# Performance work log

Measured on AMD Instinct MI355X. Metric: run time of the kernel, lower is better.

The kernel has to match this reference:

```python
import jax, jax.numpy as jnp
import numpy as np

N = 8192
E = 262144

def gcn_conv(x, W, b, row, col, w):
    # PyG GCNConv with self-loops already appended to (row, col, w).
    h = x @ W                                   # [N, out]
    deg = jax.ops.segment_sum(w, col, num_segments=N)
    dinv = jnp.where(deg > 0, jax.lax.rsqrt(deg), 0.0)
    norm = dinv[row] * w * dinv[col]            # [E+N]
    out = jax.ops.segment_sum(norm[:, None] * h[row], col, num_segments=N)
    return out + b

def setup_inputs() -> dict:
    key = jax.random.key(0)
    ks = jax.random.split(key, 10)
    return {
        "x": jax.random.normal(ks[0], (N, 512), jnp.float32),
        "edge_index": jax.random.randint(ks[1], (2, E), 0, N, jnp.int64),
        "edge_weight": jax.random.uniform(ks[2], (E,), jnp.float32),
        "noise": jax.random.normal(ks[3], (N, 64), jnp.float32),
        "W1": jax.random.normal(ks[4], (512, 256), jnp.float32) * 0.05,
        "b1": jnp.zeros((256,), jnp.float32),
        "W2": jax.random.normal(ks[5], (256, 256), jnp.float32) * 0.05,
        "b2": jnp.zeros((256,), jnp.float32),
        "Wm": jax.random.normal(ks[6], (256, 64), jnp.float32) * 0.05,
        "bm": jnp.zeros((64,), jnp.float32),
        "Ws": jax.random.normal(ks[7], (256, 64), jnp.float32) * 0.05,
        "bs": jnp.zeros((64,), jnp.float32),
    }

def reference(x, edge_index, edge_weight, noise, W1, b1, W2, b2, Wm, bm, Ws, bs):
    # add self-loops once (weight 1.0), shared by all GCN layers
    loop = jnp.arange(N, dtype=edge_index.dtype)
    row = jnp.concatenate([edge_index[0], loop])
    col = jnp.concatenate([edge_index[1], loop])
    w = jnp.concatenate([edge_weight, jnp.ones((N,), edge_weight.dtype)])

    h = jax.nn.relu(gcn_conv(x, W1, b1, row, col, w))
    h = jax.nn.relu(gcn_conv(h, W2, b2, row, col, w))
    mean = jax.nn.relu(gcn_conv(h, Wm, bm, row, col, w))
    log_std = jax.nn.relu(gcn_conv(h, Ws, bs, row, col, w))
    z = noise * jnp.exp(log_std) + mean          # [N, 64]
    adj = jax.nn.sigmoid(z @ z.T)                # [N, N]
    return jnp.triu(adj, k=1)
```

## Files before the change

### kernel.cpp

```cpp
#include <hip/hip_runtime.h>
#include <hip/hip_bf16.h>

#define NN 8192
#define NE 262144

typedef __attribute__((ext_vector_type(8))) short bf16x8;
typedef __attribute__((ext_vector_type(4))) float f32x4;

__global__ __launch_bounds__(256) void k_init(float* __restrict__ deg, int* __restrict__ counts,
                                              int* __restrict__ cnt2) {
  int i = blockIdx.x * 256 + threadIdx.x;
  if (i < NN) { deg[i] = 1.0f; counts[i] = 0; cnt2[i] = 0; }
}

__global__ __launch_bounds__(256) void k_count(const int* __restrict__ ei, const float* __restrict__ w,
                                               float* __restrict__ deg, int* __restrict__ counts) {
  int e = blockIdx.x * 256 + threadIdx.x;
  if (e < NE) {
    int c = ei[NE + e];
    atomicAdd(&deg[c], w[e]);
    atomicAdd(&counts[c], 1);
  }
}

__global__ __launch_bounds__(1024) void k_scan(const int* __restrict__ counts, int* __restrict__ offs) {
  __shared__ int part[1024];
  int t = threadIdx.x;
  int base = t * 8;
  int local[8];
  int s = 0;
#pragma unroll
  for (int j = 0; j < 8; ++j) { local[j] = counts[base + j]; s += local[j]; }
  part[t] = s;
  __syncthreads();
  for (int off = 1; off < 1024; off <<= 1) {
    int v = (t >= off) ? part[t - off] : 0;
    __syncthreads();
    part[t] += v;
    __syncthreads();
  }
  int run = (t > 0) ? part[t - 1] : 0;
#pragma unroll
  for (int j = 0; j < 8; ++j) { offs[base + j] = run; run += local[j]; }
  if (t == 1023) offs[NN] = run;
}

__global__ __launch_bounds__(256) void k_scatter(const int* __restrict__ ei, const float* __restrict__ w,
                                                 const float* __restrict__ deg, const int* __restrict__ offs,
                                                 int* __restrict__ cnt2, int* __restrict__ csr_row,
                                                 float* __restrict__ csr_val) {
  int e = blockIdx.x * 256 + threadIdx.x;
  if (e < NE) {
    int r = ei[e], c = ei[NE + e];
    int slot = offs[c] + atomicAdd(&cnt2[c], 1);
    csr_row[slot] = r;
    csr_val[slot] = rsqrtf(deg[r]) * w[e] * rsqrtf(deg[c]);
  }
}

__global__ __launch_bounds__(256) void k_gemm(const float* __restrict__ A, const float* __restrict__ B,
                                              float* __restrict__ C, int M, int K, int Nc) {
  __shared__ float As[16][68];
  __shared__ float Bs[16][64];
  int t = threadIdx.x;
  int tx = t & 15, ty = t >> 4;
  int m0 = blockIdx.y * 64, n0 = blockIdx.x * 64;
  int la_r = t >> 2;
  int la_c = (t & 3) * 4;
  int lb_r = t >> 4;
  int lb_c = (t & 15) * 4;
  const float* Aptr = A + (size_t)(m0 + la_r) * K + la_c;
  const float* Bptr = B + (size_t)lb_r * Nc + n0 + lb_c;
  float acc[4][4] = {};
  for (int k0 = 0; k0 < K; k0 += 16) {
    float4 av = *(const float4*)(Aptr + k0);
    float4 bv = *(const float4*)(Bptr + (size_t)k0 * Nc);
    __syncthreads();
    As[la_c + 0][la_r] = av.x;
    As[la_c + 1][la_r] = av.y;
    As[la_c + 2][la_r] = av.z;
    As[la_c + 3][la_r] = av.w;
    *(float4*)&Bs[lb_r][lb_c] = bv;
    __syncthreads();
#pragma unroll
    for (int kk = 0; kk < 16; ++kk) {
      f32x4 a4 = *(const f32x4*)&As[kk][ty * 4];
      f32x4 b4 = *(const f32x4*)&Bs[kk][tx * 4];
#pragma unroll
      for (int i = 0; i < 4; ++i)
#pragma unroll
        for (int j = 0; j < 4; ++j)
          acc[i][j] = fmaf(a4[i], b4[j], acc[i][j]);
    }
  }
#pragma unroll
  for (int i = 0; i < 4; ++i) {
    f32x4 v = {acc[i][0], acc[i][1], acc[i][2], acc[i][3]};
    *(f32x4*)&C[(size_t)(m0 + ty * 4 + i) * Nc + n0 + tx * 4] = v;
  }
}

template <int D>
__global__ __launch_bounds__(256) void k_agg(const float* __restrict__ t, const float* __restrict__ deg,
                                             const int* __restrict__ csr_row, const float* __restrict__ csr_val,
                                             const int* __restrict__ offs, const float* __restrict__ bias,
                                             float* __restrict__ outb) {
  constexpr int V = D / 64;
  __shared__ int   srow[256];
  __shared__ float sval[256];
  __shared__ float sacc[4][D];
  int c = blockIdx.x;
  int tid = threadIdx.x;
  int w = tid >> 6, lane = tid & 63;
  int d0 = lane * V;
  float acc[V];
#pragma unroll
  for (int j = 0; j < V; ++j) acc[j] = 0.0f;
  int s0 = offs[c], s1 = offs[c + 1];
  for (int base = s0; base < s1; base += 256) {
    int cnt = s1 - base; if (cnt > 256) cnt = 256;
    __syncthreads();
    if (tid < cnt) { srow[tid] = csr_row[base + tid]; sval[tid] = csr_val[base + tid]; }
    __syncthreads();
    for (int s = w; s < cnt; s += 4) {
      int r = srow[s];
      float v = sval[s];
      const float* p = t + (size_t)r * D + d0;
      if constexpr (V == 4) {
        float4 pv = *(const float4*)p;
        acc[0] = fmaf(v, pv.x, acc[0]);
        acc[1] = fmaf(v, pv.y, acc[1]);
        acc[2] = fmaf(v, pv.z, acc[2]);
        acc[3] = fmaf(v, pv.w, acc[3]);
      } else {
        float2 pv = *(const float2*)p;
        acc[0] = fmaf(v, pv.x, acc[0]);
        acc[1] = fmaf(v, pv.y, acc[1]);
      }
    }
  }
#pragma unroll
  for (int j = 0; j < V; ++j) sacc[w][d0 + j] = acc[j];
  __syncthreads();
  if (tid < 64) {
    float di = rsqrtf(deg[c]);
    float selfw = di * di;
#pragma unroll
    for (int j = 0; j < V; ++j) {
      int d = tid * V + j;
      float a = sacc[0][d] + sacc[1][d] + sacc[2][d] + sacc[3][d];
      a = fmaf(selfw, t[(size_t)c * D + d], a);
      outb[(size_t)c * D + d] = fmaxf(a + bias[d], 0.0f);
    }
  }
}

__global__ __launch_bounds__(256) void k_cat(const float* __restrict__ Wm, const float* __restrict__ Wsw,
                                             const float* __restrict__ bm, const float* __restrict__ bsv,
                                             float* __restrict__ Wcat, float* __restrict__ bcat) {
  int idx = blockIdx.x * 256 + threadIdx.x;
  if (idx < 256 * 128) {
    int k = idx >> 7, c = idx & 127;
    Wcat[idx] = (c < 64) ? Wm[k * 64 + c] : Wsw[k * 64 + (c - 64)];
  } else if (idx < 256 * 128 + 128) {
    int c = idx - 256 * 128;
    bcat[c] = (c < 64) ? bm[c] : bsv[c - 64];
  }
}

__global__ __launch_bounds__(256) void k_z(const float* __restrict__ gms, const float* __restrict__ noise,
                                           __hip_bfloat16* __restrict__ zh, __hip_bfloat16* __restrict__ zl) {
  int idx = blockIdx.x * 256 + threadIdx.x;
  int i = idx >> 6, k = idx & 63;
  float mean = gms[(size_t)i * 128 + k];
  float ls = gms[(size_t)i * 128 + 64 + k];
  float z = noise[idx] * __expf(ls) + mean;
  __hip_bfloat16 h = __float2bfloat16(z);
  zh[idx] = h;
  zl[idx] = __float2bfloat16(z - __bfloat162float(h));
}

__global__ __launch_bounds__(256) void k_final(const short* __restrict__ zh, const short* __restrict__ zl,
                                               float* __restrict__ out) {
  int ti = blockIdx.y, tj = blockIdx.x;
  int ri0 = ti * 128, cj0 = tj * 128;
  if (tj < ti) {
    f32x4 zz = {};
    int tr = threadIdx.x >> 5;
    int tc = (threadIdx.x & 31) << 2;
    float* base = out + (size_t)(ri0 + tr) * NN + cj0 + tc;
#pragma unroll
    for (int rr = 0; rr < 128; rr += 8)
      *(f32x4*)(base + (size_t)rr * NN) = zz;
    return;
  }
  int wv = threadIdx.x >> 6;
  int lane = threadIdx.x & 63;
  int wr = wv >> 1, wc = wv & 1;
  int lr = lane & 15;
  int lk = (lane >> 4) << 3;
  int arow = ri0 + wr * 64 + lr;
  int brow = cj0 + wc * 64 + lr;

  bf16x8 ah[4][2], al[4][2];
#pragma unroll
  for (int rb = 0; rb < 4; ++rb)
#pragma unroll
    for (int ks = 0; ks < 2; ++ks) {
      int o = (arow + rb * 16) * 64 + ks * 32 + lk;
      ah[rb][ks] = *(const bf16x8*)(zh + o);
      al[rb][ks] = *(const bf16x8*)(zl + o);
    }
  f32x4 acc[4][4] = {};
#pragma unroll
  for (int cb = 0; cb < 4; ++cb) {
    bf16x8 bh[2], bl[2];
#pragma unroll
    for (int ks = 0; ks < 2; ++ks) {
      int o = (brow + cb * 16) * 64 + ks * 32 + lk;
      bh[ks] = *(const bf16x8*)(zh + o);
      bl[ks] = *(const bf16x8*)(zl + o);
    }
#pragma unroll
    for (int rb = 0; rb < 4; ++rb) {
      f32x4 c = acc[rb][cb];
#pragma unroll
      for (int ks = 0; ks < 2; ++ks) {
        c = __builtin_amdgcn_mfma_f32_16x16x32_bf16(ah[rb][ks], bh[ks], c, 0, 0, 0);
        c = __builtin_amdgcn_mfma_f32_16x16x32_bf16(ah[rb][ks], bl[ks], c, 0, 0, 0);
        c = __builtin_amdgcn_mfma_f32_16x16x32_bf16(al[rb][ks], bh[ks], c, 0, 0, 0);
      }
      acc[rb][cb] = c;
    }
  }
  int orow = ri0 + wr * 64 + ((lane >> 4) << 2);
  int ocol = cj0 + wc * 64 + (lane & 15);
#pragma unroll
  for (int rb = 0; rb < 4; ++rb)
#pragma unroll
    for (int cb = 0; cb < 4; ++cb)
#pragma unroll
      for (int r = 0; r < 4; ++r) {
        int row = orow + rb * 16 + r;
        int col = ocol + cb * 16;
        float v = acc[rb][cb][r];
        float sg = 1.0f / (1.0f + __expf(-v));
        out[(size_t)row * NN + col] = (col > row) ? sg : 0.0f;
      }
}

extern "C" void kernel_launch(void* const* d_in, const int* in_sizes, int n_in,
                              void* d_out, int out_size, void* d_ws, size_t ws_size,
                              hipStream_t stream) {
  (void)in_sizes; (void)n_in; (void)out_size; (void)ws_size;
  const float* x     = (const float*)d_in[0];
  const int*   ei    = (const int*)d_in[1];
  const float* ew    = (const float*)d_in[2];
  const float* noise = (const float*)d_in[3];
  const float* W1    = (const float*)d_in[4];
  const float* b1    = (const float*)d_in[5];
  const float* W2    = (const float*)d_in[6];
  const float* b2    = (const float*)d_in[7];
  const float* Wm    = (const float*)d_in[8];
  const float* bm    = (const float*)d_in[9];
  const float* Wsw   = (const float*)d_in[10];
  const float* bsv   = (const float*)d_in[11];
  float* out = (float*)d_out;

  char* wsb = (char*)d_ws;
  size_t off = 0;
  auto bump = [&](size_t bytes) -> void* {
    void* p = wsb + off;
    off += (bytes + 255) & ~(size_t)255;
    return p;
  };
  float* deg     = (float*)bump((size_t)NN * 4);
  int*   counts  = (int*)bump((size_t)NN * 4);
  int*   offs    = (int*)bump((size_t)(NN + 1) * 4);
  int*   cnt2    = (int*)bump((size_t)NN * 4);
  int*   csr_row = (int*)bump((size_t)NE * 4);
  float* csr_val = (float*)bump((size_t)NE * 4);
  float* bufA    = (float*)bump((size_t)NN * 256 * 4);
  float* bufB    = (float*)bump((size_t)NN * 256 * 4);
  float* bufC    = (float*)bump((size_t)NN * 128 * 4);
  float* bufG    = (float*)bump((size_t)NN * 128 * 4);
  float* Wcat    = (float*)bump((size_t)256 * 128 * 4);
  float* bcat    = (float*)bump((size_t)128 * 4);
  __hip_bfloat16* zh = (__hip_bfloat16*)bump((size_t)NN * 64 * 2);
  __hip_bfloat16* zl = (__hip_bfloat16*)bump((size_t)NN * 64 * 2);

  k_init<<<NN / 256, 256, 0, stream>>>(deg, counts, cnt2);
  k_count<<<NE / 256, 256, 0, stream>>>(ei, ew, deg, counts);
  k_scan<<<1, 1024, 0, stream>>>(counts, offs);
  k_scatter<<<NE / 256, 256, 0, stream>>>(ei, ew, deg, offs, cnt2, csr_row, csr_val);

  k_gemm<<<dim3(4, 128), 256, 0, stream>>>(x, W1, bufA, NN, 512, 256);
  k_agg<256><<<NN, 256, 0, stream>>>(bufA, deg, csr_row, csr_val, offs, b1, bufB);
  k_gemm<<<dim3(4, 128), 256, 0, stream>>>(bufB, W2, bufA, NN, 256, 256);
  k_agg<256><<<NN, 256, 0, stream>>>(bufA, deg, csr_row, csr_val, offs, b2, bufB);
  k_cat<<<129, 256, 0, stream>>>(Wm, Wsw, bm, bsv, Wcat, bcat);
  k_gemm<<<dim3(2, 128), 256, 0, stream>>>(bufB, Wcat, bufC, NN, 256, 128);
  k_agg<128><<<NN, 256, 0, stream>>>(bufC, deg, csr_row, csr_val, offs, bcat, bufG);
  k_z<<<NN * 64 / 256, 256, 0, stream>>>(bufG, noise, zh, zl);
  k_final<<<dim3(64, 64), 256, 0, stream>>>((const short*)zh, (const short*)zl, out);
}
```

Baseline: 274.0 us.

## Replace FP32 SIMT GEMMs with split-bf16 MFMA GEMMs and fused split outputs

Replaces the shared-memory FP32 FMA GEMM with a matrix-core kernel that uses three bf16 MFMA products (hi*hi, hi*lo, lo*hi) to approximate FP32 accuracy. Inputs are pre-split into hi/lo bf16 halves: x and the weights via new split kernels, and hidden activations directly inside the aggregation epilogue. The aim is to move the GEMM FLOPs onto the matrix cores. The cost is extra split passes, double-width bf16 operand traffic, and direct global loads without LDS staging, which may underuse bandwidth. Buffers are also aliased to reuse workspace.

After: 281.8 us. +2.8%, slower.

```diff
diff --git a/kernel.cpp b/kernel.cpp
--- a/kernel.cpp
+++ b/kernel.cpp
@@ -58,53 +58,100 @@
   }
 }
 
-__global__ __launch_bounds__(256) void k_gemm(const float* __restrict__ A, const float* __restrict__ B,
-                                              float* __restrict__ C, int M, int K, int Nc) {
-  __shared__ float As[16][68];
-  __shared__ float Bs[16][64];
-  int t = threadIdx.x;
-  int tx = t & 15, ty = t >> 4;
+__global__ __launch_bounds__(256) void k_splitX(const float* __restrict__ x,
+                                                __hip_bfloat16* __restrict__ xh,
+                                                __hip_bfloat16* __restrict__ xl) {
+  size_t i = ((size_t)blockIdx.x * 256 + threadIdx.x) * 4;
+  f32x4 v = *(const f32x4*)(x + i);
+#pragma unroll
+  for (int j = 0; j < 4; ++j) {
+    __hip_bfloat16 h = __float2bfloat16(v[j]);
+    xh[i + j] = h;
+    xl[i + j] = __float2bfloat16(v[j] - __bfloat162float(h));
+  }
+}
+
+__global__ __launch_bounds__(256) void k_splitW(const float* __restrict__ W,
+                                                __hip_bfloat16* __restrict__ WhT,
+                                                __hip_bfloat16* __restrict__ WlT, int K, int Nc) {
+  int idx = blockIdx.x * 256 + threadIdx.x;
+  if (idx < K * Nc) {
+    int k = idx / Nc, n = idx - k * Nc;
+    float v = W[idx];
+    __hip_bfloat16 h = __float2bfloat16(v);
+    WhT[(size_t)n * K + k] = h;
+    WlT[(size_t)n * K + k] = __float2bfloat16(v - __bfloat162float(h));
+  }
+}
+
+__global__ __launch_bounds__(256) void k_splitWcat(const float* __restrict__ Wm, const float* __restrict__ Wsw,
+                                                   const float* __restrict__ bm, const float* __restrict__ bsv,
+                                                   __hip_bfloat16* __restrict__ WhT,
+                                                   __hip_bfloat16* __restrict__ WlT,
+                                                   float* __restrict__ bcat) {
+  int idx = blockIdx.x * 256 + threadIdx.x;
+  int n = idx >> 8, k = idx & 255;
+  float v = (n < 64) ? Wm[k * 64 + n] : Wsw[k * 64 + (n - 64)];
+  __hip_bfloat16 h = __float2bfloat16(v);
+  WhT[idx] = h;
+  WlT[idx] = __float2bfloat16(v - __bfloat162float(h));
+  if (blockIdx.x == 0 && threadIdx.x < 128)
+    bcat[threadIdx.x] = (threadIdx.x < 64) ? bm[threadIdx.x] : bsv[threadIdx.x - 64];
+}
+
+__global__ __launch_bounds__(256) void k_gemm_mfma(const short* __restrict__ Ah, const short* __restrict__ Al,
+                                                   const short* __restrict__ BhT, const short* __restrict__ BlT,
+                                                   float* __restrict__ C, int K, int Nc) {
   int m0 = blockIdx.y * 64, n0 = blockIdx.x * 64;
-  int la_r = t >> 2;
-  int la_c = (t & 3) * 4;
-  int lb_r = t >> 4;
-  int lb_c = (t & 15) * 4;
-  const float* Aptr = A + (size_t)(m0 + la_r) * K + la_c;
-  const float* Bptr = B + (size_t)lb_r * Nc + n0 + lb_c;
-  float acc[4][4] = {};
-  for (int k0 = 0; k0 < K; k0 += 16) {
-    float4 av = *(const float4*)(Aptr + k0);
-    float4 bv = *(const float4*)(Bptr + (size_t)k0 * Nc);
-    __syncthreads();
-    As[la_c + 0][la_r] = av.x;
-    As[la_c + 1][la_r] = av.y;
-    As[la_c + 2][la_r] = av.z;
-    As[la_c + 3][la_r] = av.w;
-    *(float4*)&Bs[lb_r][lb_c] = bv;
-    __syncthreads();
-#pragma unroll
-    for (int kk = 0; kk < 16; ++kk) {
-      f32x4 a4 = *(const f32x4*)&As[kk][ty * 4];
-      f32x4 b4 = *(const f32x4*)&Bs[kk][tx * 4];
-#pragma unroll
-      for (int i = 0; i < 4; ++i)
-#pragma unroll
-        for (int j = 0; j < 4; ++j)
-          acc[i][j] = fmaf(a4[i], b4[j], acc[i][j]);
-    }
-  }
-#pragma unroll
-  for (int i = 0; i < 4; ++i) {
-    f32x4 v = {acc[i][0], acc[i][1], acc[i][2], acc[i][3]};
-    *(f32x4*)&C[(size_t)(m0 + ty * 4 + i) * Nc + n0 + tx * 4] = v;
-  }
-}
-
-template <int D>
+  int wv = threadIdx.x >> 6, lane = threadIdx.x & 63;
+  int wr = wv >> 1, wc = wv & 1;
+  int lr = lane & 15, lk8 = (lane >> 4) << 3;
+  int arow = m0 + wr * 32 + lr;
+  int bcol = n0 + wc * 32 + lr;
+  f32x4 acc[2][2] = {};
+  for (int k0 = 0; k0 < K; k0 += 32) {
+    bf16x8 ah[2], al[2], bh[2], bl[2];
+#pragma unroll
+    for (int rb = 0; rb < 2; ++rb) {
+      size_t o = (size_t)(arow + rb * 16) * K + k0 + lk8;
+      ah[rb] = *(const bf16x8*)(Ah + o);
+      al[rb] = *(const bf16x8*)(Al + o);
+    }
+#pragma unroll
+    for (int cb = 0; cb < 2; ++cb) {
+      size_t o = (size_t)(bcol + cb * 16) * K + k0 + lk8;
+      bh[cb] = *(const bf16x8*)(BhT + o);
+      bl[cb] = *(const bf16x8*)(BlT + o);
+    }
+#pragma unroll
+    for (int rb = 0; rb < 2; ++rb)
+#pragma unroll
+      for (int cb = 0; cb < 2; ++cb) {
+        f32x4 c = acc[rb][cb];
+        c = __builtin_amdgcn_mfma_f32_16x16x32_bf16(ah[rb], bh[cb], c, 0, 0, 0);
+        c = __builtin_amdgcn_mfma_f32_16x16x32_bf16(ah[rb], bl[cb], c, 0, 0, 0);
+        c = __builtin_amdgcn_mfma_f32_16x16x32_bf16(al[rb], bh[cb], c, 0, 0, 0);
+        acc[rb][cb] = c;
+      }
+  }
+  int orow = m0 + wr * 32 + ((lane >> 4) << 2);
+  int ocol = n0 + wc * 32 + (lane & 15);
+#pragma unroll
+  for (int rb = 0; rb < 2; ++rb)
+#pragma unroll
+    for (int cb = 0; cb < 2; ++cb)
+#pragma unroll
+      for (int r = 0; r < 4; ++r)
+        C[(size_t)(orow + rb * 16 + r) * Nc + ocol + cb * 16] = acc[rb][cb][r];
+}
+
+template <int D, bool SPLIT>
 __global__ __launch_bounds__(256) void k_agg(const float* __restrict__ t, const float* __restrict__ deg,
                                              const int* __restrict__ csr_row, const float* __restrict__ csr_val,
                                              const int* __restrict__ offs, const float* __restrict__ bias,
-                                             float* __restrict__ outb) {
+                                             float* __restrict__ outf,
+                                             __hip_bfloat16* __restrict__ outh,
+                                             __hip_bfloat16* __restrict__ outl) {
   constexpr int V = D / 64;
   __shared__ int   srow[256];
   __shared__ float sval[256];
@@ -150,21 +197,15 @@
       int d = tid * V + j;
       float a = sacc[0][d] + sacc[1][d] + sacc[2][d] + sacc[3][d];
       a = fmaf(selfw, t[(size_t)c * D + d], a);
-      outb[(size_t)c * D + d] = fmaxf(a + bias[d], 0.0f);
-    }
-  }
-}
-
-__global__ __launch_bounds__(256) void k_cat(const float* __restrict__ Wm, const float* __restrict__ Wsw,
-                                             const float* __restrict__ bm, const float* __restrict__ bsv,
-                                             float* __restrict__ Wcat, float* __restrict__ bcat) {
-  int idx = blockIdx.x * 256 + threadIdx.x;
-  if (idx < 256 * 128) {
-    int k = idx >> 7, c = idx & 127;
-    Wcat[idx] = (c < 64) ? Wm[k * 64 + c] : Wsw[k * 64 + (c - 64)];
-  } else if (idx < 256 * 128 + 128) {
-    int c = idx - 256 * 128;
-    bcat[c] = (c < 64) ? bm[c] : bsv[c - 64];
+      a = fmaxf(a + bias[d], 0.0f);
+      if constexpr (SPLIT) {
+        __hip_bfloat16 h = __float2bfloat16(a);
+        outh[(size_t)c * D + d] = h;
+        outl[(size_t)c * D + d] = __float2bfloat16(a - __bfloat162float(h));
+      } else {
+        outf[(size_t)c * D + d] = a;
+      }
+    }
   }
 }
 
@@ -280,27 +321,44 @@
   int*   cnt2    = (int*)bump((size_t)NN * 4);
   int*   csr_row = (int*)bump((size_t)NE * 4);
   float* csr_val = (float*)bump((size_t)NE * 4);
+  __hip_bfloat16* xh = (__hip_bfloat16*)bump((size_t)NN * 512 * 2);
+  __hip_bfloat16* xl = (__hip_bfloat16*)bump((size_t)NN * 512 * 2);
   float* bufA    = (float*)bump((size_t)NN * 256 * 4);
-  float* bufB    = (float*)bump((size_t)NN * 256 * 4);
-  float* bufC    = (float*)bump((size_t)NN * 128 * 4);
-  float* bufG    = (float*)bump((size_t)NN * 128 * 4);
-  float* Wcat    = (float*)bump((size_t)256 * 128 * 4);
+  __hip_bfloat16* h1h = (__hip_bfloat16*)bump((size_t)NN * 256 * 2);
+  __hip_bfloat16* h1l = (__hip_bfloat16*)bump((size_t)NN * 256 * 2);
+  __hip_bfloat16* W1hT = (__hip_bfloat16*)bump((size_t)256 * 512 * 2);
+  __hip_bfloat16* W1lT = (__hip_bfloat16*)bump((size_t)256 * 512 * 2);
+  __hip_bfloat16* W2hT = (__hip_bfloat16*)bump((size_t)256 * 256 * 2);
+  __hip_bfloat16* W2lT = (__hip_bfloat16*)bump((size_t)256 * 256 * 2);
+  __hip_bfloat16* WchT = (__hip_bfloat16*)bump((size_t)128 * 256 * 2);
+  __hip_bfloat16* WclT = (__hip_bfloat16*)bump((size_t)128 * 256 * 2);
   float* bcat    = (float*)bump((size_t)128 * 4);
   __hip_bfloat16* zh = (__hip_bfloat16*)bump((size_t)NN * 64 * 2);
   __hip_bfloat16* zl = (__hip_bfloat16*)bump((size_t)NN * 64 * 2);
+
+  __hip_bfloat16* h2h = xh;
+  __hip_bfloat16* h2l = xl;
+  float* bufG = (float*)h1h;
 
   k_init<<<NN / 256, 256, 0, stream>>>(deg, counts, cnt2);
   k_count<<<NE / 256, 256, 0, stream>>>(ei, ew, deg, counts);
   k_scan<<<1, 1024, 0, stream>>>(counts, offs);
   k_scatter<<<NE / 256, 256, 0, stream>>>(ei, ew, deg, offs, cnt2, csr_row, csr_val);
 
-  k_gemm<<<dim3(4, 128), 256, 0, stream>>>(x, W1, bufA, NN, 512, 256);
-  k_agg<256><<<NN, 256, 0, stream>>>(bufA, deg, csr_row, csr_val, offs, b1, bufB);
-  k_gemm<<<dim3(4, 128), 256, 0, stream>>>(bufB, W2, bufA, NN, 256, 256);
-  k_agg<256><<<NN, 256, 0, stream>>>(bufA, deg, csr_row, csr_val, offs, b2, bufB);
-  k_cat<<<129, 256, 0, stream>>>(Wm, Wsw, bm, bsv, Wcat, bcat);
-  k_gemm<<<dim3(2, 128), 256, 0, stream>>>(bufB, Wcat, bufC, NN, 256, 128);
-  k_agg<128><<<NN, 256, 0, stream>>>(bufC, deg, csr_row, csr_val, offs, bcat, bufG);
+  k_splitX<<<NN * 512 / 4 / 256, 256, 0, stream>>>(x, xh, xl);
+  k_splitW<<<512, 256, 0, stream>>>(W1, W1hT, W1lT, 512, 256);
+  k_splitW<<<256, 256, 0, stream>>>(W2, W2hT, W2lT, 256, 256);
+  k_splitWcat<<<128, 256, 0, stream>>>(Wm, Wsw, bm, bsv, WchT, WclT, bcat);
+
+  k_gemm_mfma<<<dim3(4, 128), 256, 0, stream>>>((const short*)xh, (const short*)xl,
+                                                (const short*)W1hT, (const short*)W1lT, bufA, 512, 256);
+  k_agg<256, true><<<NN, 256, 0, stream>>>(bufA, deg, csr_row, csr_val, offs, b1, nullptr, h1h, h1l);
+  k_gemm_mfma<<<dim3(4, 128), 256, 0, stream>>>((const short*)h1h, (const short*)h1l,
+                                                (const short*)W2hT, (const short*)W2lT, bufA, 256, 256);
+  k_agg<256, true><<<NN, 256, 0, stream>>>(bufA, deg, csr_row, csr_val, offs, b2, nullptr, h2h, h2l);
+  k_gemm_mfma<<<dim3(2, 128), 256, 0, stream>>>((const short*)h2h, (const short*)h2l,
+                                                (const short*)WchT, (const short*)WclT, bufA, 256, 128);
+  k_agg<128, false><<<NN, 256, 0, stream>>>(bufA, deg, csr_row, csr_val, offs, bcat, bufG, nullptr, nullptr);
   k_z<<<NN * 64 / 256, 256, 0, stream>>>(bufG, noise, zh, zl);
   k_final<<<dim3(64, 64), 256, 0, stream>>>((const short*)zh, (const short*)zl, out);
 }
```
